# Kernel optimization log

Measured on AMD Instinct MI355X. Metric: run time of the kernel, lower is better.

## Reference

```python
import jax, jax.numpy as jnp
import numpy as np

LAYERS, DIM, FFN, HEADS = 2, 1024, 4096, 8
HD = DIM // HEADS          # head qk dim = 128
VD = DIM                   # v_dim (double_v_dim=False)
HV = VD // HEADS           # head v dim = 128
B, L = 2, 2048
SCALE_BASE = 512.0
EPS = 1e-5


def setup_inputs() -> dict:
    key = jax.random.key(0)
    ks = jax.random.split(key, 18)
    def rn(k, shape, s=1.0):
        return jax.random.normal(k, shape, dtype=jnp.float32) * s
    return dict(
        X=rn(ks[0], (B, L, DIM)),
        Wq=rn(ks[1], (LAYERS, HEADS, DIM, HD), 1.0 / DIM),
        Wk=rn(ks[2], (LAYERS, HEADS, DIM, HD), 1.0 / DIM),
        Wv=rn(ks[3], (LAYERS, HEADS, DIM, HV), 1.0 / DIM),
        W_G=rn(ks[4], (LAYERS, DIM, VD), 1.0 / DIM),
        W_O=rn(ks[5], (LAYERS, VD, DIM), 1.0 / DIM),
        gn_w=1.0 + 0.02 * rn(ks[6], (LAYERS, VD)),
        gn_b=0.02 * rn(ks[7], (LAYERS, VD)),
        ln1_w=1.0 + 0.02 * rn(ks[8], (LAYERS, DIM)),
        ln1_b=0.02 * rn(ks[9], (LAYERS, DIM)),
        ln2_w=1.0 + 0.02 * rn(ks[10], (LAYERS, DIM)),
        ln2_b=0.02 * rn(ks[11], (LAYERS, DIM)),
        ffn_w1=rn(ks[12], (LAYERS, DIM, FFN), DIM ** -0.5),
        ffn_b1=0.02 * rn(ks[13], (LAYERS, FFN)),
        ffn_w2=rn(ks[14], (LAYERS, FFN, DIM), FFN ** -0.5),
        ffn_b2=0.02 * rn(ks[15], (LAYERS, DIM)),
    )


def _xpos_tables(length, head_dim):
    half = head_dim // 2
    pos = jnp.arange(length, dtype=jnp.float32)
    base_scale = (jnp.arange(0, head_dim, 2, dtype=jnp.float32) + 0.4 * head_dim) / (1.4 * head_dim)
    sc = base_scale[None, :] ** (pos / SCALE_BASE)[:, None]          # [L, half]
    inv_freq = 1.0 / (10000.0 ** (jnp.arange(half, dtype=jnp.float32) / half))
    ang = pos[:, None] * inv_freq[None, :]                           # [L, half]
    return sc, jnp.sin(ang), jnp.cos(ang)


def _dup(t):
    # duplicate_interleave: [L, half] -> [L, head_dim]
    return jnp.repeat(t, 2, axis=-1)


def _rotate_every_two(x):
    x1, x2 = x[..., ::2], x[..., 1::2]
    return jnp.stack([-x2, x1], axis=-1).reshape(x.shape)


def _apply_xpos(x, sc, sin, cos, downscale):
    s = 1.0 / sc if downscale else sc
    return x * _dup(cos * s) + _rotate_every_two(x) * _dup(sin * s)


def _layernorm(x, w, b):
    mu = jnp.mean(x, axis=-1, keepdims=True)
    var = jnp.var(x, axis=-1, keepdims=True)
    return (x - mu) * jax.lax.rsqrt(var + EPS) * w + b


def _decay_matrix(length):
    gammas = jnp.asarray(1.0 - np.exp(np.linspace(np.log(1 / 32), np.log(1 / 512), HEADS)), dtype=jnp.float32)
    n = jnp.arange(length, dtype=jnp.float32)
    delta = n[:, None] - n[None, :]                                  # [L, L]
    logg = jnp.log(gammas)[:, None, None]                            # [H, 1, 1]
    return jnp.where(delta[None] >= 0, jnp.exp(logg * delta[None]), 0.0)  # [H, L, L]


def _msr(X, Wq, Wk, Wv, gn_w, gn_b, W_G, W_O, D, sc, sin, cos):
    b, l, d = X.shape
    Q = _apply_xpos(jnp.einsum('bld,hde->bhle', X, Wq), sc, sin, cos, False)
    K = _apply_xpos(jnp.einsum('bld,hde->bhle', X, Wk), sc, sin, cos, True)
    V = jnp.einsum('bld,hdv->bhlv', X, Wv)
    scores = jnp.einsum('bhle,bhme->bhlm', Q, K) * D[None]           # [B,H,L,L] decayed
    Y = jnp.einsum('bhlm,bhmv->bhlv', scores, V)                     # [B,H,L,HV]
    # GroupNorm(heads, v_dim) over per-token concatenated heads == per-head norm
    mu = jnp.mean(Y, axis=-1, keepdims=True)
    var = jnp.var(Y, axis=-1, keepdims=True)
    Yn = (Y - mu) * jax.lax.rsqrt(var + EPS)
    Yn = Yn * gn_w.reshape(HEADS, 1, HV)[None] + gn_b.reshape(HEADS, 1, HV)[None]
    Yc = jnp.transpose(Yn, (0, 2, 1, 3)).reshape(b, l, VD)
    G = X @ W_G
    gate = G * jax.nn.sigmoid(G)                                     # swish
    return (gate * Yc) @ W_O


def reference(X, Wq, Wk, Wv, W_G, W_O, gn_w, gn_b, ln1_w, ln1_b, ln2_w, ln2_b, ffn_w1, ffn_b1, ffn_w2, ffn_b2):
    l = X.shape[1]
    sc, sin, cos = _xpos_tables(l, HD)
    D = _decay_matrix(l)
    for i in range(LAYERS):
        Y = _msr(_layernorm(X, ln1_w[i], ln1_b[i]), Wq[i], Wk[i], Wv[i],
                 gn_w[i], gn_b[i], W_G[i], W_O[i], D, sc, sin, cos) + X
        h = _layernorm(Y, ln2_w[i], ln2_b[i])
        h = jax.nn.gelu(h @ ffn_w1[i] + ffn_b1[i], approximate=False)
        X = h @ ffn_w2[i] + ffn_b2[i] + Y                            # Dropout is identity in eval
    return X
```

## Files before the change

### kernel.cpp

```cpp
#include <hip/hip_runtime.h>
#include <math.h>

#define DIM 1024
#define FFN_DIM 4096
#define HEADS 8
#define HD 128
#define BB 2
#define LL 2048
#define NROWS (BB*LL)

typedef __attribute__((ext_vector_type(8))) short bf16x8;
typedef __attribute__((ext_vector_type(4))) short bf16x4;
typedef __attribute__((ext_vector_type(2))) short bf16x2;
typedef __attribute__((ext_vector_type(4))) float f32x4;

__device__ inline short f2bf(float f) {
    unsigned u = __builtin_bit_cast(unsigned, f);
    unsigned r = (u + 0x7FFFu + ((u >> 16) & 1u)) >> 16;
    return (short)r;
}
__device__ inline float bf2f(short s) {
    unsigned u = ((unsigned)(unsigned short)s) << 16;
    return __builtin_bit_cast(float, u);
}

__device__ __forceinline__ void gl_lds16(const void* g, void* l) {
    __builtin_amdgcn_global_load_lds(
        (const __attribute__((address_space(1))) unsigned int*)g,
        (__attribute__((address_space(3))) unsigned int*)l, 16, 0, 0);
}

__global__ __launch_bounds__(256) void ln_kernel_bf(
    const float* __restrict__ x, const float* __restrict__ w,
    const float* __restrict__ b, short* __restrict__ out)
{
    int row = blockIdx.x;
    int tid = threadIdx.x;
    const float* xr = x + (size_t)row * DIM;
    float4 v = *(const float4*)(xr + tid * 4);
    float s  = v.x + v.y + v.z + v.w;
    float ss = v.x*v.x + v.y*v.y + v.z*v.z + v.w*v.w;
    #pragma unroll
    for (int o = 32; o > 0; o >>= 1) { s += __shfl_down(s, o); ss += __shfl_down(ss, o); }
    __shared__ float red[10];
    int wid = tid >> 6;
    if ((tid & 63) == 0) { red[wid] = s; red[4 + wid] = ss; }
    __syncthreads();
    if (tid == 0) {
        float t  = red[0] + red[1] + red[2] + red[3];
        float t2 = red[4] + red[5] + red[6] + red[7];
        float mu  = t * (1.f / DIM);
        float var = t2 * (1.f / DIM) - mu * mu;
        red[8] = mu; red[9] = rsqrtf(var + 1e-5f);
    }
    __syncthreads();
    float mu = red[8], rs = red[9];
    float4 wv = *(const float4*)(w + tid * 4);
    float4 bv = *(const float4*)(b + tid * 4);
    bf16x4 o;
    o[0] = f2bf((v.x - mu) * rs * wv.x + bv.x);
    o[1] = f2bf((v.y - mu) * rs * wv.y + bv.y);
    o[2] = f2bf((v.z - mu) * rs * wv.z + bv.z);
    o[3] = f2bf((v.w - mu) * rs * wv.w + bv.w);
    *(bf16x4*)(out + (size_t)row * DIM + tid * 4) = o;
}

__global__ __launch_bounds__(256) void transpose_cvt(
    const float* __restrict__ in, short* __restrict__ out,
    int R, int C, size_t ibs, size_t obs)
{
    __shared__ float t[32][33];
    int bz = blockIdx.z;
    int r0 = blockIdx.y * 32, c0 = blockIdx.x * 32;
    int tx = threadIdx.x & 31, ty = threadIdx.x >> 5;
    const float* ip = in + (size_t)bz * ibs;
    short* op = out + (size_t)bz * obs;
    #pragma unroll
    for (int i = 0; i < 4; ++i)
        t[ty + i * 8][tx] = ip[(size_t)(r0 + ty + i * 8) * C + c0 + tx];
    __syncthreads();
    #pragma unroll
    for (int i = 0; i < 4; ++i)
        op[(size_t)(c0 + ty + i * 8) * R + r0 + tx] = f2bf(t[tx][ty + i * 8]);
}

__global__ __launch_bounds__(256) void vt_cvt(
    const short* __restrict__ Vb, short* __restrict__ Vt)
{
    __shared__ short t[32][34];
    int r0 = blockIdx.y * 32, c0 = blockIdx.x * 32;
    int tx = threadIdx.x & 31, ty = threadIdx.x >> 5;
    #pragma unroll
    for (int i = 0; i < 4; ++i)
        t[ty + i * 8][tx] = Vb[(size_t)(r0 + ty + i * 8) * DIM + c0 + tx];
    __syncthreads();
    int b = r0 >> 11;
    int l = (r0 & (LL - 1));
    #pragma unroll
    for (int i = 0; i < 4; ++i) {
        int c = c0 + ty + i * 8;
        int h = c >> 7, v = c & 127;
        Vt[(((size_t)(b * HEADS + h) * HD + v) << 11) + l + tx] = t[tx][ty + i * 8];
    }
}

template<int EPI, int MI, int NI, int GX>
__global__ __launch_bounds__(512, 2) void gemm_pipe(
    const short* __restrict__ A, const short* __restrict__ Bt,
    void* __restrict__ Cv, const float* __restrict__ bias,
    const float* __restrict__ R_,
    void* __restrict__ P1, void* __restrict__ P2, void* __restrict__ P3,
    int N, int K, int M)
{
    constexpr int BM = 32 * MI;
    constexpr int BN = 64 * NI;
    constexpr int LA = BM / 64;
    constexpr int LB = BN / 64;
    constexpr int NBUF = (MI == 4) ? 4 : 2;
    __shared__ __align__(16) short As[NBUF][BM * 64];
    __shared__ __align__(16) short Bs[NBUF][BN * 64];
    int tid = threadIdx.x;
    int w = tid >> 6, lane = tid & 63;
    int q = lane >> 4, lr = lane & 15;
    int wr = w >> 2, wc = w & 3;

    int id = blockIdx.y * GX + blockIdx.x;
    int xcd = id & 7, j = id >> 3;
    constexpr int rx_n = (GX >= 8) ? GX / 8 : 1;
    int tp = (GX * gridDim.y) >> 3;
    int rh = tp >> 3;
    int lbx = j & 7, lby = j >> 3;
    int rx = xcd % rx_n, ry = xcd / rx_n;
    int bm = (ry * rh + lby) * BM;
    int bn = (rx * 8 + lbx) * BN;

    int srow = tid >> 3;
    int sseg = tid & 7;

    f32x4 acc[MI][NI];
    #pragma unroll
    for (int mi = 0; mi < MI; ++mi)
        #pragma unroll
        for (int ni = 0; ni < NI; ++ni) acc[mi][ni] = (f32x4){0.f, 0.f, 0.f, 0.f};

    auto stageA = [&](int bb, int k0) {
        #pragma unroll
        for (int i = 0; i < LA; ++i) {
            int row = i * 64 + srow;
            gl_lds16(A + (size_t)(bm + row) * K + k0 + ((sseg ^ (row & 7)) << 3),
                     &As[bb][(i * 512 + tid) * 8]);
        }
    };
    auto stageB = [&](int bb, int k0) {
        #pragma unroll
        for (int i = 0; i < LB; ++i) {
            int row = i * 64 + srow;
            gl_lds16(Bt + (size_t)(bn + row) * K + k0 + ((sseg ^ (row & 7)) << 3),
                     &Bs[bb][(i * 512 + tid) * 8]);
        }
    };

    int aoff = (wr * (BM / 2) + lr) * 64;
    int boff = (wc * (BN / 4) + lr) * 64;
    int seg0 = ((q ^ (lr & 7)) << 3);
    int seg1 = (((4 + q) ^ (lr & 7)) << 3);

    auto compute_half = [&](const short* as, const short* bs, int seg) {
        bf16x8 af[MI], bfr[NI];
        #pragma unroll
        for (int mi = 0; mi < MI; ++mi)
            af[mi] = *(const bf16x8*)&as[aoff + mi * 1024 + seg];
        #pragma unroll
        for (int ni = 0; ni < NI; ++ni)
            bfr[ni] = *(const bf16x8*)&bs[boff + ni * 1024 + seg];
        __builtin_amdgcn_s_setprio(1);
        #pragma unroll
        for (int mi = 0; mi < MI; ++mi)
            #pragma unroll
            for (int ni = 0; ni < NI; ++ni)
                acc[mi][ni] = __builtin_amdgcn_mfma_f32_16x16x32_bf16(af[mi], bfr[ni], acc[mi][ni], 0, 0, 0);
        __builtin_amdgcn_s_setprio(0);
    };

    int nk = K >> 6;

    if constexpr (NBUF == 2) {
        stageA(0, 0);
        stageB(0, 0);
        #pragma unroll 1
        for (int kt = 0; kt < nk; ++kt) {
            int b = kt & 1;
            if (kt + 1 < nk) {
                stageA(b ^ 1, (kt + 1) << 6);
                if constexpr (LA == 4)
                    asm volatile("s_waitcnt vmcnt(4)\ns_barrier" ::: "memory");
                else
                    asm volatile("s_waitcnt vmcnt(2)\ns_barrier" ::: "memory");
            } else {
                asm volatile("s_waitcnt vmcnt(0)\ns_barrier" ::: "memory");
            }
            compute_half(As[b], Bs[b], seg0);
            if (kt + 1 < nk) stageB(b ^ 1, (kt + 1) << 6);
            compute_half(As[b], Bs[b], seg1);
            asm volatile("s_barrier" ::: "memory");
        }
    } else {
        #pragma unroll
        for (int d = 0; d < 3; ++d) {
            stageA(d, d << 6);
            stageB(d, d << 6);
        }
        #pragma unroll 1
        for (int kt = 0; kt < nk; ++kt) {
            int b = kt & 3;
            if (kt + 3 < nk) {
                int bb = (kt + 3) & 3;
                stageA(bb, (kt + 3) << 6);
                stageB(bb, (kt + 3) << 6);
            }
            int rem = nk - 1 - kt;
            if (rem >= 3)      asm volatile("s_waitcnt vmcnt(12)\ns_barrier" ::: "memory");
            else if (rem == 2) asm volatile("s_waitcnt vmcnt(8)\ns_barrier" ::: "memory");
            else if (rem == 1) asm volatile("s_waitcnt vmcnt(4)\ns_barrier" ::: "memory");
            else               asm volatile("s_waitcnt vmcnt(0)\ns_barrier" ::: "memory");
            compute_half(As[b], Bs[b], seg0);
            compute_half(As[b], Bs[b], seg1);
            asm volatile("s_barrier" ::: "memory");
        }
    }

    if constexpr (EPI == 4) {
        int sel = bn >> 10;
        int row_base = bm + wr * (BM / 2) + q * 4;
        int l0 = row_base & (LL - 1);
        #pragma unroll
        for (int ni = 0; ni < NI; ++ni) {
            int col = bn + wc * (BN / 4) + ni * 16 + lr;
            int cq = col & (DIM - 1);
            if (sel <= 1) {
                int jj = (col & 127) >> 1;
                float lb = log2f((2.f * jj + 51.2f) / 179.2f);
                if (sel == 1) lb = -lb;
                float invf = exp2f(-(float)jj * (13.287712379549449f / 64.f));
                float snb, cnb;
                sincosf((float)l0 * invf, &snb, &cnb);
                float scb = exp2f(lb * (float)l0 * (1.f / 512.f));
                float s1, c1, s16, c16;
                __sincosf(invf, &s1, &c1);
                __sincosf(16.f * invf, &s16, &c16);
                float st1 = exp2f(lb * (1.f / 512.f));
                float st16 = exp2f(lb * (16.f / 512.f));
                short* Ob = (short*)(sel == 0 ? Cv : P1);
                #pragma unroll
                for (int mi = 0; mi < MI; ++mi) {
                    float cr = cnb, sr = snb, sv = scb;
                    #pragma unroll
                    for (int r = 0; r < 4; ++r) {
                        float cs = cr * sv, ssn = sr * sv;
                        float v = acc[mi][ni][r];
                        float p = __shfl_xor(v, 1);
                        float o = (lr & 1) ? (v * cs + p * ssn) : (v * cs - p * ssn);
                        Ob[(size_t)(row_base + mi * 16 + r) * DIM + cq] = f2bf(o);
                        if (r < 3) {
                            float crn = cr * c1 - sr * s1;
                            sr = sr * c1 + cr * s1; cr = crn;
                            sv *= st1;
                        }
                    }
                    float cbn = cnb * c16 - snb * s16;
                    snb = snb * c16 + cnb * s16; cnb = cbn;
                    scb *= st16;
                }
            } else if (sel == 2) {
                short* Vb = (short*)P2;
                #pragma unroll
                for (int mi = 0; mi < MI; ++mi)
                    #pragma unroll
                    for (int r = 0; r < 4; ++r)
                        Vb[(size_t)(row_base + mi * 16 + r) * DIM + cq] = f2bf(acc[mi][ni][r]);
            } else {
                short* Gb = (short*)P3;
                #pragma unroll
                for (int mi = 0; mi < MI; ++mi)
                    #pragma unroll
                    for (int r = 0; r < 4; ++r)
                        Gb[(size_t)(row_base + mi * 16 + r) * DIM + cq] = f2bf(acc[mi][ni][r]);
            }
        }
        return;
    }

    float* Cf = (float*)Cv;
    short* Cs = (short*)Cv;
    #pragma unroll
    for (int ni = 0; ni < NI; ++ni) {
        int col = bn + wc * (BN / 4) + ni * 16 + lr;
        float bi = 0.f;
        if constexpr (EPI == 1 || EPI == 2) bi = bias[col];
        #pragma unroll
        for (int mi = 0; mi < MI; ++mi) {
            int row0 = bm + wr * (BM / 2) + mi * 16 + q * 4;
            #pragma unroll
            for (int r = 0; r < 4; ++r) {
                size_t off = (size_t)(row0 + r) * M + col;
                float v = acc[mi][ni][r];
                if constexpr (EPI == 1) {
                    v += bi;
                    v = 0.5f * v * (1.f + erff(v * 0.70710678118654752f));
                    Cs[off] = f2bf(v);
                } else if constexpr (EPI == 2) {
                    Cf[off] = v + bi + R_[off];
                } else if constexpr (EPI == 3) {
                    Cf[off] = v + R_[off];
                } else {
                    Cf[off] = v;
                }
            }
        }
    }
}

#define PSTR 40
__global__ __launch_bounds__(512, 2) void retention_mfma2(
    const short* __restrict__ Qb, const short* __restrict__ Kb,
    const short* __restrict__ Vt, float* __restrict__ Y)
{
    __shared__ __align__(16) short Ks[2][64 * 128];
    __shared__ __align__(16) short Vs[2][128 * 64];
    __shared__ __align__(16) short Ps[8][16 * PSTR];
    int tid = threadIdx.x;
    int w = tid >> 6, lane = tid & 63;
    int q = lane >> 4, lr = lane & 15;
    int g = w >> 2;
    int qw = w & 3;
    int bh = blockIdx.x;
    int b = bh >> 3, h = bh & 7;
    size_t bL = (size_t)b * LL;
    const short* Kbh = Kb + (bL << 10) + (h << 7);
    const short* Qbh = Qb + (bL << 10) + (h << 7);
    const short* Vbh = Vt + ((size_t)bh << 18);
    float* Ybh = Y + (bL << 10) + (h << 7);

    const float lg_lo = -3.4657359027997265f;
    const float lg_hi = -6.2383246250395075f;
    float gamma = 1.f - expf(lg_lo + (lg_hi - lg_lo) * ((float)h / 7.f));
    float logg = logf(gamma);
    float gm64 = expf(-64.f * logg);
    float rf[4];
    #pragma unroll
    for (int r = 0; r < 4; ++r) rf[r] = expf(logg * (float)(q * 4 + r));
    float cf0 = expf(-logg * (float)lr);
    float cf1 = expf(-logg * (float)(16 + lr));
    int dqlr = q * 4 - lr;

    int kr_l = lane >> 4;
    int ks_l = lane & 15;
    int vr_l = lane >> 3;
    int vs_l = lane & 7;

    auto stageKV = [&](int bb, int m0) {
        #pragma unroll
        for (int i = 0; i < 2; ++i) {
            int ch = w * 2 + i;
            int kr = ch * 4 + kr_l;
            gl_lds16(Kbh + ((size_t)(m0 + kr) << 10) + ((ks_l ^ (kr & 15)) << 3),
                     &Ks[bb][ch * 512]);
            int vr = ch * 8 + vr_l;
            gl_lds16(Vbh + ((size_t)vr << 11) + m0 + ((vs_l ^ (vr & 7)) << 3),
                     &Vs[bb][ch * 512]);
        }
    };

    #pragma unroll 1
    for (int pass = 0; pass < 2; ++pass) {
        int jt = pass ? (31 - blockIdx.y) : blockIdx.y;
        int l0w = jt * 64 + qw * 16;
        int ns = jt + 1;

        bf16x8 qf[4];
        {
            const short* qp = Qbh + ((size_t)(l0w + lr) << 10) + q * 8;
            #pragma unroll
            for (int es = 0; es < 4; ++es) qf[es] = *(const bf16x8*)(qp + es * 32);
        }
        f32x4 yacc[8];
        #pragma unroll
        for (int vt = 0; vt < 8; ++vt) yacc[vt] = (f32x4){0.f, 0.f, 0.f, 0.f};
        float tf = expf(logg * (float)(l0w - g * 32));

        stageKV(0, 0);

        #pragma unroll 1
        for (int s = 0; s < ns; ++s) {
            int buf = s & 1;
            if (s + 1 < ns) {
                stageKV(buf ^ 1, (s + 1) * 64);
                asm volatile("s_waitcnt vmcnt(4)\ns_barrier" ::: "memory");
            } else {
                asm volatile("s_waitcnt vmcnt(0)\ns_barrier" ::: "memory");
            }
            int m0 = s * 64 + g * 32;
            if (m0 <= l0w + 15) {
                int dt = l0w - m0;
                const short* ksub = &Ks[buf][g * 32 * 128];
                f32x4 sa0 = (f32x4){0.f,0.f,0.f,0.f};
                f32x4 sa1 = (f32x4){0.f,0.f,0.f,0.f};
                #pragma unroll
                for (int es = 0; es < 4; ++es) {
                    int slot = ((es * 4 + q) ^ lr) * 8;
                    bf16x8 bk0 = *(const bf16x8*)&ksub[lr * 128 + slot];
                    bf16x8 bk1 = *(const bf16x8*)&ksub[(16 + lr) * 128 + slot];
                    sa0 = __builtin_amdgcn_mfma_f32_16x16x32_bf16(qf[es], bk0, sa0, 0, 0, 0);
                    sa1 = __builtin_amdgcn_mfma_f32_16x16x32_bf16(qf[es], bk1, sa1, 0, 0, 0);
                }
                #pragma unroll
                for (int r = 0; r < 4; ++r) {
                    float p0 = sa0[r] * (rf[r] * cf0 * tf);
                    float p1 = sa1[r] * (rf[r] * cf1 * tf);
                    int d0 = dt + dqlr + r;
                    Ps[w][(q*4 + r) * PSTR + lr]      = (d0 >= 0)      ? f2bf(p0) : (short)0;
                    Ps[w][(q*4 + r) * PSTR + 16 + lr] = (d0 - 16 >= 0) ? f2bf(p1) : (short)0;
                }
                bf16x8 pa = *(const bf16x8*)&Ps[w][lr * PSTR + q * 8];
                #pragma unroll
                for (int vt = 0; vt < 8; ++vt) {
                    bf16x8 bv = *(const bf16x8*)&Vs[buf][(vt * 16 + lr) * 64 + (((g * 4 + q) ^ (lr & 7)) << 3)];
                    yacc[vt] = __builtin_amdgcn_mfma_f32_16x16x32_bf16(pa, bv, yacc[vt], 0, 0, 0);
                }
            }
            tf *= gm64;
            asm volatile("s_barrier" ::: "memory");
        }
        __syncthreads();
        float* sc = (float*)&Ks[0][0] + qw * 2048;
        if (g) {
            #pragma unroll
            for (int vt = 0; vt < 8; ++vt)
                #pragma unroll
                for (int r = 0; r < 4; ++r)
                    sc[(q * 4 + r) * 128 + ((vt * 16 + lr) ^ (q * 8))] = yacc[vt][r];
        }
        __syncthreads();
        if (!g) {
            float* yp = Ybh + ((size_t)(l0w + q * 4) << 10) + lr;
            #pragma unroll
            for (int vt = 0; vt < 8; ++vt)
                #pragma unroll
                for (int r = 0; r < 4; ++r)
                    yp[((size_t)r << 10) + vt * 16] =
                        yacc[vt][r] + sc[(q * 4 + r) * 128 + ((vt * 16 + lr) ^ (q * 8))];
        }
        __syncthreads();
    }
}

__global__ __launch_bounds__(256) void gn_gate_kernel(
    const float* __restrict__ Y, const short* __restrict__ Gb,
    const float* __restrict__ w, const float* __restrict__ b,
    short* __restrict__ ybf)
{
    int tid = threadIdx.x;
    int wid = tid >> 6, lane = tid & 63;
    int grp = blockIdx.x * 4 + wid;
    int n = grp >> 3, h = grp & 7;
    size_t base = (size_t)n * DIM + h * HD + lane * 2;
    float2 y = *(const float2*)(Y + base);
    float s = y.x + y.y, ss = y.x * y.x + y.y * y.y;
    #pragma unroll
    for (int o = 32; o > 0; o >>= 1) { s += __shfl_down(s, o); ss += __shfl_down(ss, o); }
    s = __shfl(s, 0); ss = __shfl(ss, 0);
    float mu  = s * (1.f / HD);
    float var = ss * (1.f / HD) - mu * mu;
    float rs  = rsqrtf(var + 1e-5f);
    float2 wv = *(const float2*)(w + h * HD + lane * 2);
    float2 bv = *(const float2*)(b + h * HD + lane * 2);
    bf16x2 gv = *(const bf16x2*)(Gb + base);
    float gx = bf2f(gv[0]), gy = bf2f(gv[1]);
    float g0 = gx / (1.f + expf(-gx));
    float g1 = gy / (1.f + expf(-gy));
    bf16x2 o;
    o[0] = f2bf(((y.x - mu) * rs * wv.x + bv.x) * g0);
    o[1] = f2bf(((y.y - mu) * rs * wv.y + bv.y) * g1);
    *(bf16x2*)(ybf + base) = o;
}

extern "C" void kernel_launch(void* const* d_in, const int* in_sizes, int n_in,
                              void* d_out, int out_size, void* d_ws, size_t ws_size,
                              hipStream_t stream)
{
    const float* X0   = (const float*)d_in[0];
    const float* Wq   = (const float*)d_in[1];
    const float* Wk   = (const float*)d_in[2];
    const float* Wv   = (const float*)d_in[3];
    const float* WG   = (const float*)d_in[4];
    const float* WO   = (const float*)d_in[5];
    const float* gnw  = (const float*)d_in[6];
    const float* gnb  = (const float*)d_in[7];
    const float* ln1w = (const float*)d_in[8];
    const float* ln1b = (const float*)d_in[9];
    const float* ln2w = (const float*)d_in[10];
    const float* ln2b = (const float*)d_in[11];
    const float* fw1  = (const float*)d_in[12];
    const float* fb1  = (const float*)d_in[13];
    const float* fw2  = (const float*)d_in[14];
    const float* fb2  = (const float*)d_in[15];

    float* ws = (float*)d_ws;
    const size_t U = (size_t)NROWS * DIM;

    short* lnbf  = (short*)(ws + 0 * U);
    short* wqkvg = lnbf + (size_t)NROWS * DIM;
    short* Vt   = (short*)(ws + 1 * U);
    short* fw1t = (short*)(ws + 1 * U);
    short* fw2t = fw1t + (size_t)DIM * FFN_DIM;
    float* sY  = ws + 2 * U;
    short* h1   = (short*)(ws + 2 * U);
    short* Vb   = (short*)(ws + 3 * U);
    short* ybf  = (short*)(ws + 3 * U);
    short* wot  = ybf + (size_t)NROWS * DIM;
    short* Gb   = (short*)(ws + 4 * U);
    float* sXn = ws + 4 * U;
    short* Qb   = (short*)(ws + 5 * U);
    short* Kb   = Qb + (size_t)NROWS * DIM;
    float* sX  = ws + 6 * U;

    for (int i = 0; i < 2; ++i) {
        const float* Xin = (i == 0) ? X0 : sX;
        float* Xout = (i == 1) ? (float*)d_out : sX;

        ln_kernel_bf<<<NROWS, 256, 0, stream>>>(Xin, ln1w + i * DIM, ln1b + i * DIM, lnbf);
        dim3 tq(HD / 32, DIM / 32, HEADS);
        transpose_cvt<<<tq, 256, 0, stream>>>(Wq + (size_t)i * HEADS * DIM * HD, wqkvg + 0 * DIM * DIM, DIM, HD, (size_t)DIM * HD, (size_t)HD * DIM);
        transpose_cvt<<<tq, 256, 0, stream>>>(Wk + (size_t)i * HEADS * DIM * HD, wqkvg + 1 * DIM * DIM, DIM, HD, (size_t)DIM * HD, (size_t)HD * DIM);
        transpose_cvt<<<tq, 256, 0, stream>>>(Wv + (size_t)i * HEADS * DIM * HD, wqkvg + 2 * DIM * DIM, DIM, HD, (size_t)DIM * HD, (size_t)HD * DIM);
        dim3 tg(DIM / 32, DIM / 32, 1);
        transpose_cvt<<<tg, 256, 0, stream>>>(WG + (size_t)i * DIM * DIM, wqkvg + 3 * (size_t)DIM * DIM, DIM, DIM, 0, 0);
        dim3 gp4(4 * DIM / 256, NROWS / 256);
        gemm_pipe<4, 8, 4, 16><<<gp4, 512, 0, stream>>>(lnbf, wqkvg, Qb, nullptr, nullptr, Kb, Vb, Gb, NROWS, DIM, 4 * DIM);
        dim3 vg(DIM / 32, NROWS / 32);
        vt_cvt<<<vg, 256, 0, stream>>>(Vb, Vt);
        dim3 rg(16, 16);
        retention_mfma2<<<rg, 512, 0, stream>>>(Qb, Kb, Vt, sY);
        gn_gate_kernel<<<NROWS * HEADS / 4, 256, 0, stream>>>(sY, Gb, gnw + i * DIM, gnb + i * DIM, ybf);
        transpose_cvt<<<tg, 256, 0, stream>>>(WO + (size_t)i * DIM * DIM, wot, DIM, DIM, 0, 0);
        dim3 gp(DIM / 128, NROWS / 128);
        gemm_pipe<3, 4, 2, 8><<<gp, 512, 0, stream>>>(ybf, wot, sXn, nullptr, Xin, nullptr, nullptr, nullptr, NROWS, DIM, DIM);
        ln_kernel_bf<<<NROWS, 256, 0, stream>>>(sXn, ln2w + i * DIM, ln2b + i * DIM, lnbf);
        dim3 t1(FFN_DIM / 32, DIM / 32, 1);
        transpose_cvt<<<t1, 256, 0, stream>>>(fw1 + (size_t)i * DIM * FFN_DIM, fw1t, DIM, FFN_DIM, 0, 0);
        dim3 t2(DIM / 32, FFN_DIM / 32, 1);
        transpose_cvt<<<t2, 256, 0, stream>>>(fw2 + (size_t)i * FFN_DIM * DIM, fw2t, FFN_DIM, DIM, 0, 0);
        dim3 gf1(FFN_DIM / 256, NROWS / 256);
        gemm_pipe<1, 8, 4, 16><<<gf1, 512, 0, stream>>>(lnbf, fw1t, h1, fb1 + i * FFN_DIM, nullptr, nullptr, nullptr, nullptr, NROWS, DIM, FFN_DIM);
        dim3 gf2(DIM / 128, NROWS / 128);
        gemm_pipe<2, 4, 2, 8><<<gf2, 512, 0, stream>>>(h1, fw2t, Xout, fb2 + i * DIM, sXn, nullptr, nullptr, nullptr, NROWS, FFN_DIM, DIM);
    }
}
```

Measured before the change: 723.4 us.

## Add specialized MI=8 GEMM path with k-half split LDS layout and finer pipelining

```diff
diff --git a/kernel.cpp b/kernel.cpp
--- a/kernel.cpp
+++ b/kernel.cpp
@@ -114,8 +114,6 @@
 {
     constexpr int BM = 32 * MI;
     constexpr int BN = 64 * NI;
-    constexpr int LA = BM / 64;
-    constexpr int LB = BN / 64;
     constexpr int NBUF = (MI == 4) ? 4 : 2;
     __shared__ __align__(16) short As[NBUF][BM * 64];
     __shared__ __align__(16) short Bs[NBUF][BN * 64];
@@ -134,77 +132,144 @@
     int bm = (ry * rh + lby) * BM;
     int bn = (rx * 8 + lbx) * BN;
 
-    int srow = tid >> 3;
-    int sseg = tid & 7;
-
     f32x4 acc[MI][NI];
     #pragma unroll
     for (int mi = 0; mi < MI; ++mi)
         #pragma unroll
         for (int ni = 0; ni < NI; ++ni) acc[mi][ni] = (f32x4){0.f, 0.f, 0.f, 0.f};
 
-    auto stageA = [&](int bb, int k0) {
-        #pragma unroll
-        for (int i = 0; i < LA; ++i) {
-            int row = i * 64 + srow;
-            gl_lds16(A + (size_t)(bm + row) * K + k0 + ((sseg ^ (row & 7)) << 3),
-                     &As[bb][(i * 512 + tid) * 8]);
-        }
-    };
-    auto stageB = [&](int bb, int k0) {
-        #pragma unroll
-        for (int i = 0; i < LB; ++i) {
-            int row = i * 64 + srow;
-            gl_lds16(Bt + (size_t)(bn + row) * K + k0 + ((sseg ^ (row & 7)) << 3),
-                     &Bs[bb][(i * 512 + tid) * 8]);
-        }
-    };
-
-    int aoff = (wr * (BM / 2) + lr) * 64;
-    int boff = (wc * (BN / 4) + lr) * 64;
-    int seg0 = ((q ^ (lr & 7)) << 3);
-    int seg1 = (((4 + q) ^ (lr & 7)) << 3);
-
-    auto compute_half = [&](const short* as, const short* bs, int seg) {
-        bf16x8 af[MI], bfr[NI];
-        #pragma unroll
-        for (int mi = 0; mi < MI; ++mi)
-            af[mi] = *(const bf16x8*)&as[aoff + mi * 1024 + seg];
-        #pragma unroll
-        for (int ni = 0; ni < NI; ++ni)
-            bfr[ni] = *(const bf16x8*)&bs[boff + ni * 1024 + seg];
-        __builtin_amdgcn_s_setprio(1);
-        #pragma unroll
-        for (int mi = 0; mi < MI; ++mi)
-            #pragma unroll
-            for (int ni = 0; ni < NI; ++ni)
-                acc[mi][ni] = __builtin_amdgcn_mfma_f32_16x16x32_bf16(af[mi], bfr[ni], acc[mi][ni], 0, 0, 0);
-        __builtin_amdgcn_s_setprio(0);
-    };
-
     int nk = K >> 6;
 
-    if constexpr (NBUF == 2) {
-        stageA(0, 0);
-        stageB(0, 0);
+    if constexpr (MI == 8) {
+        int segoff = (q ^ ((lr >> 1) & 3)) << 3;
+
+        auto stageAh = [&](int bb, int kglob, int kh) {
+            #pragma unroll
+            for (int i = 0; i < 2; ++i) {
+                int c = i * 512 + tid;
+                int row = c >> 2, seg = c & 3;
+                gl_lds16(A + (size_t)(bm + row) * K + kglob + ((seg ^ ((row >> 1) & 3)) << 3),
+                         &As[bb][kh * 8192 + c * 8]);
+            }
+        };
+        auto stageBh = [&](int bb, int kglob, int kh) {
+            #pragma unroll
+            for (int i = 0; i < 2; ++i) {
+                int c = i * 512 + tid;
+                int row = c >> 2, seg = c & 3;
+                gl_lds16(Bt + (size_t)(bn + row) * K + kglob + ((seg ^ ((row >> 1) & 3)) << 3),
+                         &Bs[bb][kh * 8192 + c * 8]);
+            }
+        };
+        auto ldA = [&](int b, int kh, int ma, bf16x8* af) {
+            #pragma unroll
+            for (int mi = 0; mi < 4; ++mi)
+                af[mi] = *(const bf16x8*)&As[b][kh * 8192 +
+                         (wr * 128 + ma * 64 + mi * 16 + lr) * 32 + segoff];
+        };
+        auto ldB = [&](int b, int kh, bf16x8* bq) {
+            #pragma unroll
+            for (int ni = 0; ni < 4; ++ni)
+                bq[ni] = *(const bf16x8*)&Bs[b][kh * 8192 +
+                         (wc * 64 + ni * 16 + lr) * 32 + segoff];
+        };
+
+        stageAh(0, 0, 0); stageBh(0, 0, 0); stageAh(0, 32, 1); stageBh(0, 32, 1);
+        asm volatile("s_waitcnt vmcnt(4)\ns_barrier" ::: "memory");
+
         #pragma unroll 1
         for (int kt = 0; kt < nk; ++kt) {
             int b = kt & 1;
-            if (kt + 1 < nk) {
-                stageA(b ^ 1, (kt + 1) << 6);
-                if constexpr (LA == 4)
-                    asm volatile("s_waitcnt vmcnt(4)\ns_barrier" ::: "memory");
-                else
-                    asm volatile("s_waitcnt vmcnt(2)\ns_barrier" ::: "memory");
-            } else {
-                asm volatile("s_waitcnt vmcnt(0)\ns_barrier" ::: "memory");
-            }
-            compute_half(As[b], Bs[b], seg0);
-            if (kt + 1 < nk) stageB(b ^ 1, (kt + 1) << 6);
-            compute_half(As[b], Bs[b], seg1);
-            asm volatile("s_barrier" ::: "memory");
+            int kn = (kt + 1) << 6;
+            bool pf = (kt + 1 < nk);
+            bf16x8 af[4], bq[4];
+            ldB(b, 0, bq); ldA(b, 0, 0, af);
+            if (pf) stageAh(b ^ 1, kn, 0);
+            asm volatile("s_barrier" ::: "memory");
+            __builtin_amdgcn_s_setprio(1);
+            #pragma unroll
+            for (int mi = 0; mi < 4; ++mi)
+                #pragma unroll
+                for (int ni = 0; ni < 4; ++ni)
+                    acc[mi][ni] = __builtin_amdgcn_mfma_f32_16x16x32_bf16(af[mi], bq[ni], acc[mi][ni], 0, 0, 0);
+            __builtin_amdgcn_s_setprio(0);
+            asm volatile("s_barrier" ::: "memory");
+            ldA(b, 0, 1, af);
+            if (pf) stageBh(b ^ 1, kn, 0);
+            asm volatile("s_barrier" ::: "memory");
+            __builtin_amdgcn_s_setprio(1);
+            #pragma unroll
+            for (int mi = 0; mi < 4; ++mi)
+                #pragma unroll
+                for (int ni = 0; ni < 4; ++ni)
+                    acc[4 + mi][ni] = __builtin_amdgcn_mfma_f32_16x16x32_bf16(af[mi], bq[ni], acc[4 + mi][ni], 0, 0, 0);
+            __builtin_amdgcn_s_setprio(0);
+            if (pf) asm volatile("s_waitcnt vmcnt(4)\ns_barrier" ::: "memory");
+            else    asm volatile("s_waitcnt vmcnt(0)\ns_barrier" ::: "memory");
+            ldB(b, 1, bq); ldA(b, 1, 0, af);
+            if (pf) stageAh(b ^ 1, kn + 32, 1);
+            asm volatile("s_barrier" ::: "memory");
+            __builtin_amdgcn_s_setprio(1);
+            #pragma unroll
+            for (int mi = 0; mi < 4; ++mi)
+                #pragma unroll
+                for (int ni = 0; ni < 4; ++ni)
+                    acc[mi][ni] = __builtin_amdgcn_mfma_f32_16x16x32_bf16(af[mi], bq[ni], acc[mi][ni], 0, 0, 0);
+            __builtin_amdgcn_s_setprio(0);
+            asm volatile("s_barrier" ::: "memory");
+            ldA(b, 1, 1, af);
+            if (pf) stageBh(b ^ 1, kn + 32, 1);
+            asm volatile("s_barrier" ::: "memory");
+            __builtin_amdgcn_s_setprio(1);
+            #pragma unroll
+            for (int mi = 0; mi < 4; ++mi)
+                #pragma unroll
+                for (int ni = 0; ni < 4; ++ni)
+                    acc[4 + mi][ni] = __builtin_amdgcn_mfma_f32_16x16x32_bf16(af[mi], bq[ni], acc[4 + mi][ni], 0, 0, 0);
+            __builtin_amdgcn_s_setprio(0);
+            if (pf) asm volatile("s_waitcnt vmcnt(4)\ns_barrier" ::: "memory");
+            else    asm volatile("s_barrier" ::: "memory");
         }
     } else {
+        int srow = tid >> 3;
+        int sseg = tid & 7;
+        auto stageA = [&](int bb, int k0) {
+            #pragma unroll
+            for (int i = 0; i < BM / 64; ++i) {
+                int row = i * 64 + srow;
+                gl_lds16(A + (size_t)(bm + row) * K + k0 + ((sseg ^ (row & 7)) << 3),
+                         &As[bb][(i * 512 + tid) * 8]);
+            }
+        };
+        auto stageB = [&](int bb, int k0) {
+            #pragma unroll
+            for (int i = 0; i < BN / 64; ++i) {
+                int row = i * 64 + srow;
+                gl_lds16(Bt + (size_t)(bn + row) * K + k0 + ((sseg ^ (row & 7)) << 3),
+                         &Bs[bb][(i * 512 + tid) * 8]);
+            }
+        };
+        int aoff = (wr * (BM / 2) + lr) * 64;
+        int boff = (wc * (BN / 4) + lr) * 64;
+        int seg0 = ((q ^ (lr & 7)) << 3);
+        int seg1 = (((4 + q) ^ (lr & 7)) << 3);
+        auto compute_half = [&](const short* as, const short* bs, int seg) {
+            bf16x8 af[MI], bfr[NI];
+            #pragma unroll
+            for (int mi = 0; mi < MI; ++mi)
+                af[mi] = *(const bf16x8*)&as[aoff + mi * 1024 + seg];
+            #pragma unroll
+            for (int ni = 0; ni < NI; ++ni)
+                bfr[ni] = *(const bf16x8*)&bs[boff + ni * 1024 + seg];
+            __builtin_amdgcn_s_setprio(1);
+            #pragma unroll
+            for (int mi = 0; mi < MI; ++mi)
+                #pragma unroll
+                for (int ni = 0; ni < NI; ++ni)
+                    acc[mi][ni] = __builtin_amdgcn_mfma_f32_16x16x32_bf16(af[mi], bfr[ni], acc[mi][ni], 0, 0, 0);
+            __builtin_amdgcn_s_setprio(0);
+        };
+
         #pragma unroll
         for (int d = 0; d < 3; ++d) {
             stageA(d, d << 6);
```

Measured after the change: 725.8 us. No clear change (+0.3%).
